# Kernel tuning notes

Hardware: AMD Instinct MI355X
Metric: run time of the kernel (lower is better)

## Reference

```python
import jax, jax.numpy as jnp
import numpy as np

B, N, DIN, DOUT = 8, 2048, 256, 256

def setup_inputs() -> dict:
    key = jax.random.key(0)
    k1, k2, k3 = jax.random.split(key, 3)
    H = jax.random.normal(k1, (B, N, DIN), dtype=jnp.float32)
    G = jax.random.uniform(k2, (B, N, N), dtype=jnp.float32)  # positive -> nonzero row/col sums
    # xavier_uniform-style scale for the weight
    limit = float(np.sqrt(6.0 / (DIN + DOUT)))
    W = jax.random.uniform(k3, (DIN, DOUT), dtype=jnp.float32, minval=-limit, maxval=limit)
    return {"H": H, "G": G, "W": W}

def reference(H, G, W):
    # N_e = H @ W : [b,n,dout]
    N_e = H @ W
    # symmetric part
    G_F = (G + jnp.swapaxes(G, 1, 2)) * 0.5
    # loop over k of outer products == two normalized Gram matrices:
    # G_Sin[i,j] = sum_k G[k,i]*G[k,j] / rowsum_k  == G^T diag(1/rowsum) G
    # G_So[i,j]  = sum_k G[i,k]*G[j,k] / colsum_k  == G diag(1/colsum) G^T
    rs = G.sum(axis=-1)  # [b,n] row sums
    cs = G.sum(axis=-2)  # [b,n] col sums
    G_Sin = jnp.einsum('bki,bkj->bij', G / rs[:, :, None], G)
    G_So = jnp.einsum('bik,bjk->bij', G / cs[:, None, :], G)
    H_out = jnp.concatenate([
        jax.nn.relu(G_F @ N_e),
        jax.nn.relu(G_Sin @ N_e),
        jax.nn.relu(G_So @ N_e),
    ], axis=-1)  # [b,n,3*dout]
    return H_out
```

## Files before the change

### kernel.cpp

```cpp
#include <hip/hip_runtime.h>
#include <hip/hip_bf16.h>


constexpr int NN = 2048;
constexpr long GSTR = (long)NN * NN;

using frag8   = __attribute__((ext_vector_type(8))) short;
using floatx4 = __attribute__((ext_vector_type(4))) float;
using ush8    = __attribute__((ext_vector_type(8))) unsigned short;

__device__ inline unsigned short f2bf(float x) {
    unsigned u = __float_as_uint(x);
    u += 0x7FFF + ((u >> 16) & 1);
    return (unsigned short)(u >> 16);
}
__device__ inline float bf2f(unsigned short h) {
    return __uint_as_float((unsigned)h << 16);
}
__device__ inline ushort2 pk2(float a, float b) {
    union { __hip_bfloat162 h; ushort2 u; } cv;
    cv.h = __float22bfloat162_rn(float2{a, b});
    return cv.u;
}
__device__ inline void gload_lds16(const void* g, void* l) {
    __builtin_amdgcn_global_load_lds(
        (const __attribute__((address_space(1))) void*)g,
        (__attribute__((address_space(3))) void*)l, 16, 0, 0);
}

enum { EPI_NE = 0, EPI_M1 = 1, EPI_P2 = 2, EPI_O3 = 3 };
enum { A_F32ROW = 0, A_DMA = 1 };

template <int EPI, int AMODE, int TM, int WJ, int NJ>
__global__ __launch_bounds__(256) void mgemm(
    const void* __restrict__ Aptr,
    const unsigned short* __restrict__ B0,
    const unsigned short* __restrict__ B1,
    const float* __restrict__ rsraw,
    unsigned short* __restrict__ CsT,
    float* __restrict__ outp,
    const float* __restrict__ scale,
    int K, int lda, long strideA, long sB)
{
    constexpr int MF = TM / 32;
    constexpr int NF = WJ / 32;
    __shared__ __align__(16) unsigned short As[TM * 64];
    __shared__ __align__(16) unsigned short Bs[WJ * 64];

    const int t  = threadIdx.x;
    const int bx = blockIdx.x;
    const int xcd = bx & 7;
    const int kk  = bx >> 3;
    constexpr int PER = NJ * 8;
    const int itile = xcd + 8 * (kk / PER);
    const int rem   = kk & (PER - 1);
    const int bb    = rem / NJ;
    const int jt    = rem & (NJ - 1);
    const int i0b = itile * TM;
    const int j0  = jt * WJ;

    const unsigned short* Btb =
        ((EPI == EPI_P2 && j0 >= 256) ? B1 + (long)(j0 - 256) * K
                                      : B0 + (long)j0 * K) + (long)bb * sB;

    const int w = t >> 6, l = t & 63;
    const int wm = w >> 1, wn = w & 1;
    const int quad = l >> 4, c15 = l & 15;

    const int lr  = l >> 3, ls = l & 7;

    floatx4 acc[MF][NF] = {};

    for (int k0 = 0; k0 < K; k0 += 64) {
        if constexpr (AMODE == A_DMA) {
            const unsigned short* Au = (const unsigned short*)Aptr
                + (long)bb * strideA
                + (((long)itile * (K >> 7) + (k0 >> 7)) << 14);
            const int kin = k0 & 127;
            #pragma unroll
            for (int q = 0; q < TM / 32; ++q) {
                const int rt = q * 32 + w * 8;
                gload_lds16(Au + (rt + lr) * 128 + kin + ((ls ^ lr) << 3),
                            &As[rt * 64]);
            }
        } else {
            const float* Af = (const float*)Aptr + (long)bb * strideA;
            const int ar  = t >> 2;
            const int ac0 = (t & 3) * 2;
            const float* ap = Af + (long)(i0b + ar) * lda + k0 + ac0 * 8;
            const float4 x0 = *(const float4*)(ap + 0);
            const float4 x1 = *(const float4*)(ap + 4);
            const float4 x2 = *(const float4*)(ap + 8);
            const float4 x3 = *(const float4*)(ap + 12);
            union { ush8 v; ushort2 u2[4]; } p0, p1;
            p0.u2[0] = pk2(x0.x, x0.y); p0.u2[1] = pk2(x0.z, x0.w);
            p0.u2[2] = pk2(x1.x, x1.y); p0.u2[3] = pk2(x1.z, x1.w);
            p1.u2[0] = pk2(x2.x, x2.y); p1.u2[1] = pk2(x2.z, x2.w);
            p1.u2[2] = pk2(x3.x, x3.y); p1.u2[3] = pk2(x3.z, x3.w);
            const int sw = ar & 7;
            *(ush8*)&As[ar * 64 + ((ac0 ^ sw) << 3)]       = p0.v;
            *(ush8*)&As[ar * 64 + (((ac0 + 1) ^ sw) << 3)] = p1.v;
        }
        #pragma unroll
        for (int q = 0; q < WJ / 32; ++q) {
            const int rt = q * 32 + w * 8;
            gload_lds16(Btb + (long)(rt + lr) * K + k0 + ((ls ^ lr) << 3),
                        &Bs[rt * 64]);
        }
        __syncthreads();

        #pragma unroll
        for (int ks = 0; ks < 2; ++ks) {
            frag8 af[MF], bfv[NF];
            const int swr = c15 & 7;
            #pragma unroll
            for (int mt = 0; mt < MF; ++mt)
                af[mt] = *(const frag8*)&As[(wm * (TM / 2) + mt * 16 + c15) * 64
                                            + (((ks * 4 + quad) ^ swr) << 3)];
            #pragma unroll
            for (int nt = 0; nt < NF; ++nt)
                bfv[nt] = *(const frag8*)&Bs[(wn * (WJ / 2) + nt * 16 + c15) * 64
                                             + (((ks * 4 + quad) ^ swr) << 3)];
            #pragma unroll
            for (int mt = 0; mt < MF; ++mt)
                #pragma unroll
                for (int nt = 0; nt < NF; ++nt)
                    acc[mt][nt] = __builtin_amdgcn_mfma_f32_16x16x32_bf16(
                        af[mt], bfv[nt], acc[mt][nt], 0, 0, 0);
        }
        __syncthreads();
    }

    const long rowb = (long)bb * NN;
    #pragma unroll
    for (int mt = 0; mt < MF; ++mt) {
        const int il = wm * (TM / 2) + mt * 16 + quad * 4;
        const int ib = i0b + il;
        float4 s4 = make_float4(1.f, 1.f, 1.f, 1.f);
        if constexpr (EPI == EPI_M1) s4 = *(const float4*)(scale + rowb + ib);
        if constexpr (EPI == EPI_P2) {
            if (j0 < 256) s4 = *(const float4*)(scale + rowb + ib);
        }
        #pragma unroll
        for (int nt = 0; nt < NF; ++nt) {
            floatx4 v = acc[mt][nt];
            const int gj = j0 + wn * (WJ / 2) + nt * 16 + c15;
            if constexpr (EPI == EPI_NE) {
                union { ushort4 v; ushort2 u2[2]; } p;
                p.u2[0] = pk2(v[0], v[1]); p.u2[1] = pk2(v[2], v[3]);
                *(ushort4*)(CsT + ((long)bb * 256 + gj) * 2048 + ib) = p.v;
            } else if constexpr (EPI == EPI_M1) {
                union { ushort4 v; ushort2 u2[2]; } p;
                p.u2[0] = pk2(v[0] * s4.x, v[1] * s4.y);
                p.u2[1] = pk2(v[2] * s4.z, v[3] * s4.w);
                *(ushort4*)(CsT + ((long)bb * 256 + gj) * 2048 + ib) = p.v;
            } else if constexpr (EPI == EPI_P2) {
                if (j0 < 256) {
                    union { ushort4 v; ushort2 u2[2]; } p;
                    p.u2[0] = pk2(v[0] * s4.x, v[1] * s4.y);
                    p.u2[1] = pk2(v[2] * s4.z, v[3] * s4.w);
                    *(ushort4*)(CsT + ((long)bb * 256 + gj) * 2048 + ib) = p.v;
                    const float4 rr = *(const float4*)(rsraw + rowb + ib);
                    const ushort4 m1p = *(const ushort4*)(B1 + ((long)bb * 256 + gj) * 2048 + ib);
                    const float m1v[4] = {bf2f(m1p.x) * rr.x, bf2f(m1p.y) * rr.y,
                                          bf2f(m1p.z) * rr.z, bf2f(m1p.w) * rr.w};
                    #pragma unroll
                    for (int r = 0; r < 4; ++r)
                        outp[(rowb + ib + r) * 768 + gj] = fmaxf(0.5f * (v[r] + m1v[r]), 0.f);
                } else {
                    #pragma unroll
                    for (int r = 0; r < 4; ++r)
                        outp[(rowb + ib + r) * 768 + gj] = fmaxf(v[r], 0.f);
                }
            } else {
                #pragma unroll
                for (int r = 0; r < 4; ++r)
                    outp[(rowb + ib + r) * 768 + 512 + gj] = fmaxf(v[r], 0.f);
            }
        }
    }
}

__global__ __launch_bounds__(256) void cvt_stream(
    const float* __restrict__ G,
    unsigned short* __restrict__ Gbf,
    float* __restrict__ pcs,
    float* __restrict__ inv_rs, float* __restrict__ rs_raw)
{
    __shared__ float sm[4][16];
    const int b  = blockIdx.y;
    const int s  = blockIdx.x;
    const int i0 = s * 16;
    const int t  = threadIdx.x;
    const int c8 = t * 8;
    const int w  = t >> 6, l = t & 63;

    const float* gp = G + (long)b * GSTR + (long)i0 * NN + c8;
    unsigned short* gb = Gbf + (long)b * GSTR;
    const int tc = c8 >> 7, cin = c8 & 127;

    float csum[8] = {};
    float rp[16];

    #pragma unroll
    for (int r = 0; r < 16; ++r) {
        const float4 x0 = *(const float4*)(gp + (long)r * NN);
        const float4 x1 = *(const float4*)(gp + (long)r * NN + 4);
        union { ush8 v; ushort2 u2[4]; } pk;
        pk.u2[0] = pk2(x0.x, x0.y); pk.u2[1] = pk2(x0.z, x0.w);
        pk.u2[2] = pk2(x1.x, x1.y); pk.u2[3] = pk2(x1.z, x1.w);
        const int gi = i0 + r;
        *(ush8*)(gb + (((long)(gi >> 7) * 16 + tc) << 14) + ((gi & 127) << 7) + cin) = pk.v;
        rp[r] = x0.x + x0.y + x0.z + x0.w + x1.x + x1.y + x1.z + x1.w;
        csum[0] += x0.x; csum[1] += x0.y; csum[2] += x0.z; csum[3] += x0.w;
        csum[4] += x1.x; csum[5] += x1.y; csum[6] += x1.z; csum[7] += x1.w;
    }

    float* pp = pcs + ((long)b * 128 + s) * NN + c8;
    *(float4*)pp       = make_float4(csum[0], csum[1], csum[2], csum[3]);
    *(float4*)(pp + 4) = make_float4(csum[4], csum[5], csum[6], csum[7]);

    #pragma unroll
    for (int r = 0; r < 16; ++r) {
        rp[r] += __shfl_xor(rp[r], 1);
        rp[r] += __shfl_xor(rp[r], 2);
        rp[r] += __shfl_xor(rp[r], 4);
        rp[r] += __shfl_xor(rp[r], 8);
        rp[r] += __shfl_xor(rp[r], 16);
        rp[r] += __shfl_xor(rp[r], 32);
    }
    if (l == 0) {
        #pragma unroll
        for (int r = 0; r < 16; ++r) sm[w][r] = rp[r];
    }
    __syncthreads();
    if (t < 16) {
        const float s_ = sm[0][t] + sm[1][t] + sm[2][t] + sm[3][t];
        rs_raw[(long)b * NN + i0 + t] = s_;
        inv_rs[(long)b * NN + i0 + t] = 1.0f / s_;
    }
}

__global__ __launch_bounds__(256) void cvt_t(
    const unsigned short* __restrict__ Gbf, unsigned short* __restrict__ GbfT)
{
    const int b  = blockIdx.z;
    const int tr = blockIdx.y, tc = blockIdx.x;
    const long src = (long)b * GSTR + (((long)tr * 16 + tc) << 14);
    const long dst = (long)b * GSTR + (((long)tc * 16 + tr) << 14);
    const int t = threadIdx.x;
    const int w = t >> 6, l = t & 63;
    const int wm = w >> 1, wn = w & 1;
    const int rg = l >> 3, c = l & 7;
    const int il = wm * 64 + rg * 8;
    const int jl = wn * 64 + c * 8;

    union RowU { ush8 v; unsigned u4[4]; };
    RowU rows[8], cols[8];
    #pragma unroll
    for (int r = 0; r < 8; ++r)
        rows[r].v = *(const ush8*)(Gbf + src + (long)(il + r) * 128 + jl);
    __builtin_amdgcn_sched_barrier(0);

    #pragma unroll
    for (int p = 0; p < 4; ++p) {
        #pragma unroll
        for (int k = 0; k < 4; ++k) {
            const unsigned a = rows[2 * p].u4[k], bq = rows[2 * p + 1].u4[k];
            cols[2 * k].u4[p]     = (a & 0xffffu) | (bq << 16);
            cols[2 * k + 1].u4[p] = (a >> 16) | (bq & 0xffff0000u);
        }
    }
    #pragma unroll
    for (int j = 0; j < 8; ++j)
        *(ush8*)(GbfT + dst + (long)(jl + j) * 128 + il) = cols[j].v;
}

__global__ __launch_bounds__(256) void finalize(
    const float* __restrict__ pcs,
    float* __restrict__ inv_cs,
    const float* __restrict__ W, unsigned short* __restrict__ Wt)
{
    const int idx = blockIdx.x * 256 + threadIdx.x;
    if (blockIdx.y == 0) {
        const int b = idx >> 11, i = idx & 2047;
        float s = 0.f;
        for (int ic = 0; ic < 128; ++ic) s += pcs[((long)b * 128 + ic) * NN + i];
        inv_cs[idx] = 1.0f / s;
    } else {
        #pragma unroll
        for (int e = 0; e < 4; ++e) {
            const int flat = idx * 4 + e;
            const int j = flat >> 8, k = flat & 255;
            Wt[flat] = f2bf(W[(long)k * 256 + j]);
        }
    }
}

extern "C" void kernel_launch(void* const* d_in, const int* in_sizes, int n_in,
                              void* d_out, int out_size, void* d_ws, size_t ws_size,
                              hipStream_t stream)
{
    constexpr int B = 8;
    const float* H = (const float*)d_in[0];
    const float* G = (const float*)d_in[1];
    const float* W = (const float*)d_in[2];
    float* out = (float*)d_out;

    unsigned short* ws16 = (unsigned short*)d_ws;
    unsigned short* Gbf  = ws16;
    unsigned short* GbfT = Gbf  + (long)B * GSTR;
    unsigned short* Wt   = GbfT + (long)B * GSTR;
    unsigned short* NeT  = Wt   + 65536;
    unsigned short* M1sT = NeT  + 4194304;
    unsigned short* M2sT = M1sT + 4194304;
    float* inv_rs = (float*)(M2sT + 4194304);
    float* rs_raw = inv_rs + 16384;
    float* inv_cs = rs_raw + 16384;
    float* pcs    = inv_cs + 16384;

    cvt_stream<<<dim3(128, 8), 256, 0, stream>>>(G, Gbf, pcs, inv_rs, rs_raw);
    cvt_t<<<dim3(16, 16, 8), 256, 0, stream>>>(Gbf, GbfT);
    finalize<<<dim3(64, 2), 256, 0, stream>>>(pcs, inv_cs, W, Wt);

    const long sNT = 256L * NN;
    mgemm<EPI_NE, A_F32ROW, 64, 64, 4><<<1024, 256, 0, stream>>>(
        H, Wt, nullptr, nullptr, NeT, nullptr, nullptr,
        256, 256, 2048L * 256, 0);
    mgemm<EPI_M1, A_DMA, 128, 64, 4><<<512, 256, 0, stream>>>(
        Gbf, NeT, nullptr, nullptr, M1sT, nullptr, inv_rs,
        2048, 2048, GSTR, sNT);
    mgemm<EPI_P2, A_DMA, 128, 128, 4><<<512, 256, 0, stream>>>(
        GbfT, NeT, M1sT, rs_raw, M2sT, out, inv_cs,
        2048, 2048, GSTR, sNT);
    mgemm<EPI_O3, A_DMA, 128, 64, 4><<<512, 256, 0, stream>>>(
        Gbf, M2sT, nullptr, nullptr, nullptr, out, nullptr,
        2048, 2048, GSTR, sNT);
}
```

Baseline: 374.9 us.

## Double-buffer LDS tiles in GEMM and pre-convert H to tiled bf16

The GEMM main loop now uses two LDS buffers per operand. It issues the DMA loads for the next K tile before computing on the current one, so the global-to-LDS latency overlaps with MFMA work, and it keeps one barrier per iteration instead of two. H is converted once to bf16 in the same 128-column tiled layout as G by a new kernel, which removes the fp32 load-and-convert path inside the GEMM. The N_e GEMM then uses 128-row tiles. The cost is double the LDS per block, which may lower occupancy, plus an extra kernel launch and workspace buffer.

```diff
diff --git a/kernel.cpp b/kernel.cpp
--- a/kernel.cpp
+++ b/kernel.cpp
@@ -29,23 +29,22 @@
 }
 
 enum { EPI_NE = 0, EPI_M1 = 1, EPI_P2 = 2, EPI_O3 = 3 };
-enum { A_F32ROW = 0, A_DMA = 1 };
-
-template <int EPI, int AMODE, int TM, int WJ, int NJ>
+
+template <int EPI, int TM, int WJ, int NJ>
 __global__ __launch_bounds__(256) void mgemm(
-    const void* __restrict__ Aptr,
+    const unsigned short* __restrict__ Aptr,
     const unsigned short* __restrict__ B0,
     const unsigned short* __restrict__ B1,
     const float* __restrict__ rsraw,
     unsigned short* __restrict__ CsT,
     float* __restrict__ outp,
     const float* __restrict__ scale,
-    int K, int lda, long strideA, long sB)
+    int K, long strideA, long sB)
 {
     constexpr int MF = TM / 32;
     constexpr int NF = WJ / 32;
-    __shared__ __align__(16) unsigned short As[TM * 64];
-    __shared__ __align__(16) unsigned short Bs[WJ * 64];
+    __shared__ __align__(16) unsigned short As[2][TM * 64];
+    __shared__ __align__(16) unsigned short Bs[2][WJ * 64];
 
     const int t  = threadIdx.x;
     const int bx = blockIdx.x;
@@ -62,6 +61,7 @@
     const unsigned short* Btb =
         ((EPI == EPI_P2 && j0 >= 256) ? B1 + (long)(j0 - 256) * K
                                       : B0 + (long)j0 * K) + (long)bb * sB;
+    const unsigned short* Ab = Aptr + (long)bb * strideA;
 
     const int w = t >> 6, l = t & 63;
     const int wm = w >> 1, wn = w & 1;
@@ -71,43 +71,34 @@
 
     floatx4 acc[MF][NF] = {};
 
-    for (int k0 = 0; k0 < K; k0 += 64) {
-        if constexpr (AMODE == A_DMA) {
-            const unsigned short* Au = (const unsigned short*)Aptr
-                + (long)bb * strideA
-                + (((long)itile * (K >> 7) + (k0 >> 7)) << 14);
-            const int kin = k0 & 127;
-            #pragma unroll
-            for (int q = 0; q < TM / 32; ++q) {
-                const int rt = q * 32 + w * 8;
-                gload_lds16(Au + (rt + lr) * 128 + kin + ((ls ^ lr) << 3),
-                            &As[rt * 64]);
-            }
-        } else {
-            const float* Af = (const float*)Aptr + (long)bb * strideA;
-            const int ar  = t >> 2;
-            const int ac0 = (t & 3) * 2;
-            const float* ap = Af + (long)(i0b + ar) * lda + k0 + ac0 * 8;
-            const float4 x0 = *(const float4*)(ap + 0);
-            const float4 x1 = *(const float4*)(ap + 4);
-            const float4 x2 = *(const float4*)(ap + 8);
-            const float4 x3 = *(const float4*)(ap + 12);
-            union { ush8 v; ushort2 u2[4]; } p0, p1;
-            p0.u2[0] = pk2(x0.x, x0.y); p0.u2[1] = pk2(x0.z, x0.w);
-            p0.u2[2] = pk2(x1.x, x1.y); p0.u2[3] = pk2(x1.z, x1.w);
-            p1.u2[0] = pk2(x2.x, x2.y); p1.u2[1] = pk2(x2.z, x2.w);
-            p1.u2[2] = pk2(x3.x, x3.y); p1.u2[3] = pk2(x3.z, x3.w);
-            const int sw = ar & 7;
-            *(ush8*)&As[ar * 64 + ((ac0 ^ sw) << 3)]       = p0.v;
-            *(ush8*)&As[ar * 64 + (((ac0 + 1) ^ sw) << 3)] = p1.v;
+    const int NT = K >> 6;
+
+    auto stage = [&](int buf, int k0) {
+        const unsigned short* Au = Ab + (((long)itile * (K >> 7) + (k0 >> 7)) << 14);
+        const int kin = k0 & 127;
+        #pragma unroll
+        for (int q = 0; q < TM / 32; ++q) {
+            const int rt = q * 32 + w * 8;
+            gload_lds16(Au + (rt + lr) * 128 + kin + ((ls ^ lr) << 3),
+                        &As[buf][rt * 64]);
         }
         #pragma unroll
         for (int q = 0; q < WJ / 32; ++q) {
             const int rt = q * 32 + w * 8;
             gload_lds16(Btb + (long)(rt + lr) * K + k0 + ((ls ^ lr) << 3),
-                        &Bs[rt * 64]);
-        }
-        __syncthreads();
+                        &Bs[buf][rt * 64]);
+        }
+    };
+
+    stage(0, 0);
+    asm volatile("s_waitcnt vmcnt(0)" ::: "memory");
+    __builtin_amdgcn_s_barrier();
+    __builtin_amdgcn_sched_barrier(0);
+
+    int cur = 0;
+    for (int tt = 0; tt < NT; ++tt) {
+        if (tt + 1 < NT) stage(cur ^ 1, (tt + 1) << 6);
+        __builtin_amdgcn_sched_barrier(0);
 
         #pragma unroll
         for (int ks = 0; ks < 2; ++ks) {
@@ -115,12 +106,12 @@
             const int swr = c15 & 7;
             #pragma unroll
             for (int mt = 0; mt < MF; ++mt)
-                af[mt] = *(const frag8*)&As[(wm * (TM / 2) + mt * 16 + c15) * 64
-                                            + (((ks * 4 + quad) ^ swr) << 3)];
+                af[mt] = *(const frag8*)&As[cur][(wm * (TM / 2) + mt * 16 + c15) * 64
+                                               + (((ks * 4 + quad) ^ swr) << 3)];
             #pragma unroll
             for (int nt = 0; nt < NF; ++nt)
-                bfv[nt] = *(const frag8*)&Bs[(wn * (WJ / 2) + nt * 16 + c15) * 64
-                                             + (((ks * 4 + quad) ^ swr) << 3)];
+                bfv[nt] = *(const frag8*)&Bs[cur][(wn * (WJ / 2) + nt * 16 + c15) * 64
+                                                + (((ks * 4 + quad) ^ swr) << 3)];
             #pragma unroll
             for (int mt = 0; mt < MF; ++mt)
                 #pragma unroll
@@ -128,7 +119,13 @@
                     acc[mt][nt] = __builtin_amdgcn_mfma_f32_16x16x32_bf16(
                         af[mt], bfv[nt], acc[mt][nt], 0, 0, 0);
         }
-        __syncthreads();
+
+        if (tt + 1 < NT) {
+            asm volatile("s_waitcnt vmcnt(0)" ::: "memory");
+            __builtin_amdgcn_s_barrier();
+            __builtin_amdgcn_sched_barrier(0);
+        }
+        cur ^= 1;
     }
 
     const long rowb = (long)bb * NN;
@@ -276,6 +273,27 @@
         *(ush8*)(GbfT + dst + (long)(jl + j) * 128 + il) = cols[j].v;
 }
 
+__global__ __launch_bounds__(256) void cvt_h(
+    const float* __restrict__ H, unsigned short* __restrict__ Hbf)
+{
+    const int b = blockIdx.y, it = blockIdx.x;
+    const int t = threadIdx.x;
+    const int rsub = t >> 5, c = (t & 31) * 8;
+    const float* hp = H + ((long)b * 2048 + (long)it * 128) * 256;
+    unsigned short* ob = Hbf + (long)b * (2048L * 256) + (((long)it * 2 + (c >> 7)) << 14);
+    const int cin = c & 127;
+    #pragma unroll
+    for (int rr = 0; rr < 16; ++rr) {
+        const int r = rr * 8 + rsub;
+        const float4 x0 = *(const float4*)(hp + (long)r * 256 + c);
+        const float4 x1 = *(const float4*)(hp + (long)r * 256 + c + 4);
+        union { ush8 v; ushort2 u2[4]; } pk;
+        pk.u2[0] = pk2(x0.x, x0.y); pk.u2[1] = pk2(x0.z, x0.w);
+        pk.u2[2] = pk2(x1.x, x1.y); pk.u2[3] = pk2(x1.z, x1.w);
+        *(ush8*)(ob + r * 128 + cin) = pk.v;
+    }
+}
+
 __global__ __launch_bounds__(256) void finalize(
     const float* __restrict__ pcs,
     float* __restrict__ inv_cs,
@@ -314,26 +332,28 @@
     unsigned short* NeT  = Wt   + 65536;
     unsigned short* M1sT = NeT  + 4194304;
     unsigned short* M2sT = M1sT + 4194304;
-    float* inv_rs = (float*)(M2sT + 4194304);
+    unsigned short* Hbf  = M2sT + 4194304;
+    float* inv_rs = (float*)(Hbf + 4194304);
     float* rs_raw = inv_rs + 16384;
     float* inv_cs = rs_raw + 16384;
     float* pcs    = inv_cs + 16384;
 
     cvt_stream<<<dim3(128, 8), 256, 0, stream>>>(G, Gbf, pcs, inv_rs, rs_raw);
     cvt_t<<<dim3(16, 16, 8), 256, 0, stream>>>(Gbf, GbfT);
+    cvt_h<<<dim3(16, 8), 256, 0, stream>>>(H, Hbf);
     finalize<<<dim3(64, 2), 256, 0, stream>>>(pcs, inv_cs, W, Wt);
 
     const long sNT = 256L * NN;
-    mgemm<EPI_NE, A_F32ROW, 64, 64, 4><<<1024, 256, 0, stream>>>(
-        H, Wt, nullptr, nullptr, NeT, nullptr, nullptr,
-        256, 256, 2048L * 256, 0);
-    mgemm<EPI_M1, A_DMA, 128, 64, 4><<<512, 256, 0, stream>>>(
+    mgemm<EPI_NE, 128, 64, 4><<<512, 256, 0, stream>>>(
+        Hbf, Wt, nullptr, nullptr, NeT, nullptr, nullptr,
+        256, 2048L * 256, 0);
+    mgemm<EPI_M1, 128, 64, 4><<<512, 256, 0, stream>>>(
         Gbf, NeT, nullptr, nullptr, M1sT, nullptr, inv_rs,
-        2048, 2048, GSTR, sNT);
-    mgemm<EPI_P2, A_DMA, 128, 128, 4><<<512, 256, 0, stream>>>(
+        2048, GSTR, sNT);
+    mgemm<EPI_P2, 128, 128, 4><<<512, 256, 0, stream>>>(
         GbfT, NeT, M1sT, rs_raw, M2sT, out, inv_cs,
-        2048, 2048, GSTR, sNT);
-    mgemm<EPI_O3, A_DMA, 128, 64, 4><<<512, 256, 0, stream>>>(
+        2048, GSTR, sNT);
+    mgemm<EPI_O3, 128, 64, 4><<<512, 256, 0, stream>>>(
         Gbf, M2sT, nullptr, nullptr, nullptr, out, nullptr,
-        2048, 2048, GSTR, sNT);
-}
+        2048, GSTR, sNT);
+}
```

Result: no change. 373.7 us (-0.3%).
